# Kernel tuning notes

Hardware: AMD Instinct MI355X
Metric: run time of the kernel (lower is better)

The kernel has to match this reference:

```python
import jax, jax.numpy as jnp
import numpy as np

N = 50000
IN_C, HID_C, CLS_C = 512, 256, 128
E = 800000


def setup_inputs() -> dict:
    key = jax.random.key(0)
    k1, k2, k3, k4, k5, k6 = jax.random.split(key, 6)
    x = jax.random.normal(k1, (N, IN_C), dtype=jnp.float32)
    edge_index = jax.random.randint(k2, (2, E), 0, N, dtype=jnp.int64)
    # GCNConv params (glorot weights, zero bias as in PyG init)
    W1 = jax.random.normal(k3, (IN_C, HID_C), dtype=jnp.float32) * (1.0 / np.sqrt(IN_C))
    b1 = jnp.zeros((HID_C,), dtype=jnp.float32)
    W2 = jax.random.normal(k4, (HID_C, CLS_C), dtype=jnp.float32) * (1.0 / np.sqrt(HID_C))
    b2 = jnp.zeros((CLS_C,), dtype=jnp.float32)
    return {"x": x, "W1": W1, "b1": b1, "W2": W2, "b2": b2, "edge_index": edge_index}


def _norm_edges(edge_index, n):
    # PyG GCNConv: add self-loops, symmetric normalization deg^-1/2
    loops = jnp.arange(n, dtype=edge_index.dtype)
    src = jnp.concatenate([edge_index[0], loops])
    dst = jnp.concatenate([edge_index[1], loops])
    ones = jnp.ones_like(src, dtype=jnp.float32)
    deg = jax.ops.segment_sum(ones, dst, num_segments=n)
    dinv = jnp.where(deg > 0, jax.lax.rsqrt(deg), 0.0)
    norm = dinv[src] * dinv[dst]  # [E+N]
    return src, dst, norm


def _gcn_conv(x, W, b, src, dst, norm, n):
    h = x @ W  # project first (out_channels < in_channels)
    msg = h[src] * norm[:, None]  # gather + scale, [E+N, C]
    out = jax.ops.segment_sum(msg, dst, num_segments=n)  # scatter-add
    return out + b


def reference(x, W1, b1, W2, b2, edge_index):
    n = x.shape[0]
    src, dst, norm = _norm_edges(edge_index, n)
    h = jax.nn.relu(_gcn_conv(x, W1, b1, src, dst, norm, n))
    # dropout p=0.5 is a no-op in eval mode
    out = _gcn_conv(h, W2, b2, src, dst, norm, n)
    return jax.nn.sigmoid(out)
```

## Files before the change

### kernel.cpp

```cpp
#include <hip/hip_runtime.h>

typedef __attribute__((ext_vector_type(8))) short bf16x8;
typedef __attribute__((ext_vector_type(4))) float f32x4;
typedef unsigned short u16;
typedef unsigned int u32;
typedef __attribute__((address_space(1))) const u32 gu32;
typedef __attribute__((address_space(3))) u32 lu32;

__device__ __forceinline__ float bf2f(u16 u) {
  union { u32 i; float f; } c; c.i = ((u32)u) << 16; return c.f;
}
__device__ __forceinline__ u16 f2bf(float f) {
  union { float f; u32 i; } c; c.f = f;
  u32 u = c.i;
  u32 r = (u + 0x7FFFu + ((u >> 16) & 1u)) >> 16;
  return (u16)r;
}

__device__ __forceinline__ void gld16(const void* g, void* l) {
  __builtin_amdgcn_global_load_lds((gu32*)g, (lu32*)l, 16, 0, 0);
}


__global__ void k_init_deg(int* deg, int n) {
  int i = blockIdx.x * 256 + threadIdx.x;
  if (i < n) deg[i] = 1;
}

__global__ void k_count(const int* __restrict__ ei, int* deg, int E) {
  int e = blockIdx.x * 256 + threadIdx.x;
  if (e < E) atomicAdd(&deg[ei[E + e]], 1);
}

__global__ void k_blocksum(const int* __restrict__ deg, int* bsum, int n) {
  __shared__ int s[256];
  int t = threadIdx.x;
  int i = blockIdx.x * 256 + t;
  s[t] = (i < n) ? (deg[i] - 1) : 0;
  __syncthreads();
  for (int o = 128; o > 0; o >>= 1) {
    if (t < o) s[t] += s[t + o];
    __syncthreads();
  }
  if (t == 0) bsum[blockIdx.x] = s[0];
}

__global__ void k_scanb(const int* __restrict__ bsum, int* bofs, int nb) {
  __shared__ int s[256];
  int t = threadIdx.x;
  int v = (t < nb) ? bsum[t] : 0;
  s[t] = v;
  __syncthreads();
  for (int o = 1; o < 256; o <<= 1) {
    int x = (t >= o) ? s[t - o] : 0;
    __syncthreads();
    s[t] += x;
    __syncthreads();
  }
  bofs[t] = s[t] - v;
}

__global__ void k_rowptr(const int* __restrict__ deg, const int* __restrict__ bofs,
                         int* rowptr, int* cursor, float* dinv, int n) {
  __shared__ int s[256];
  int t = threadIdx.x;
  int i = blockIdx.x * 256 + t;
  int d = (i < n) ? deg[i] : 1;
  int v = (i < n) ? (d - 1) : 0;
  s[t] = v;
  __syncthreads();
  for (int o = 1; o < 256; o <<= 1) {
    int x = (t >= o) ? s[t - o] : 0;
    __syncthreads();
    s[t] += x;
    __syncthreads();
  }
  int excl = s[t] - v + bofs[blockIdx.x];
  if (i < n) {
    rowptr[i] = excl;
    cursor[i] = excl;
    dinv[i] = rsqrtf((float)d);
    if (i == n - 1) rowptr[n] = excl + v;
  }
}

__global__ void k_fill(const int* __restrict__ ei, int* cursor,
                       const float* __restrict__ dinv, int2* colw, int E) {
  int e = blockIdx.x * 256 + threadIdx.x;
  if (e >= E) return;
  int s = ei[e];
  int d = ei[E + e];
  int pos = atomicAdd(&cursor[d], 1);
  colw[pos] = make_int2(s, __float_as_int(dinv[s]));
}

__global__ void k_twt(const float* __restrict__ W, u16* __restrict__ Wt, int K, int N) {
  int i = blockIdx.x * 256 + threadIdx.x;
  if (i >= K * N) return;
  int k = i / N, n = i - k * N;
  Wt[n * K + k] = f2bf(W[i]);
}


template <bool AF32, int K, int BM>
__launch_bounds__(256, 4)
__global__ void gemm_kernel(const void* __restrict__ Ap, const u16* __restrict__ Bt,
                            u16* __restrict__ C, int M, int ldc) {
  constexpr int NT = K / 32;
  constexpr int AE = BM * 32;
  constexpr int WROWS = BM / 2;
  constexpr int FI = WROWS / 16;
  constexpr int NJA = BM / 64;
  __shared__ u16 As_[2][AE];
  __shared__ u16 Bs_[2][4096];

  const int tid = threadIdx.x;
  const int lane = tid & 63;
  const int wid = tid >> 6;
  const int wr = wid >> 1, wc = wid & 1;
  const long brow = (long)blockIdx.x * BM;
  const long bcol = (long)blockIdx.y * 128;

  const u16* bgp[2];
  u16* blp[2];
#pragma unroll
  for (int j = 0; j < 2; ++j) {
    int idx = j * 256 + tid;
    int row = idx >> 2;
    int u = (idx & 3) ^ (row & 3);
    bgp[j] = Bt + (bcol + row) * (long)K + u * 8;
    blp[j] = &Bs_[0][idx * 8];
  }

  const float* apf = nullptr;
  int arow = 0, au0 = 0, au1 = 0;
  const u16* agp[NJA];
  u16* alp[NJA];
  if constexpr (AF32) {
    arow = tid >> 1;
    int khalf = tid & 1;
    long grow = brow + arow; if (grow > (long)M - 1) grow = M - 1;
    apf = (const float*)Ap + grow * (long)K + khalf * 16;
    int sw = arow & 3;
    au0 = (2 * khalf) ^ sw;
    au1 = (2 * khalf + 1) ^ sw;
  } else {
#pragma unroll
    for (int j = 0; j < NJA; ++j) {
      int idx = j * 256 + tid;
      int row = idx >> 2;
      int u = (idx & 3) ^ (row & 3);
      long grow = brow + row; if (grow > (long)M - 1) grow = M - 1;
      agp[j] = (const u16*)Ap + grow * (long)K + u * 8;
      alp[j] = &As_[0][idx * 8];
    }
  }

  float4 fa[4];
  auto loadA = [&](int kt) {
    const float4* p = (const float4*)(apf + kt * 32);
#pragma unroll
    for (int i = 0; i < 4; ++i) fa[i] = p[i];
  };
  auto writeA = [&](int buf) {
    union { u32 w[8]; uint4 v[2]; } pk;
    asm("v_cvt_pk_bf16_f32 %0, %1, %2" : "=v"(pk.w[0]) : "v"(fa[0].x), "v"(fa[0].y));
    asm("v_cvt_pk_bf16_f32 %0, %1, %2" : "=v"(pk.w[1]) : "v"(fa[0].z), "v"(fa[0].w));
    asm("v_cvt_pk_bf16_f32 %0, %1, %2" : "=v"(pk.w[2]) : "v"(fa[1].x), "v"(fa[1].y));
    asm("v_cvt_pk_bf16_f32 %0, %1, %2" : "=v"(pk.w[3]) : "v"(fa[1].z), "v"(fa[1].w));
    asm("v_cvt_pk_bf16_f32 %0, %1, %2" : "=v"(pk.w[4]) : "v"(fa[2].x), "v"(fa[2].y));
    asm("v_cvt_pk_bf16_f32 %0, %1, %2" : "=v"(pk.w[5]) : "v"(fa[2].z), "v"(fa[2].w));
    asm("v_cvt_pk_bf16_f32 %0, %1, %2" : "=v"(pk.w[6]) : "v"(fa[3].x), "v"(fa[3].y));
    asm("v_cvt_pk_bf16_f32 %0, %1, %2" : "=v"(pk.w[7]) : "v"(fa[3].z), "v"(fa[3].w));
    *(uint4*)&As_[buf][arow * 32 + au0 * 8] = pk.v[0];
    *(uint4*)&As_[buf][arow * 32 + au1 * 8] = pk.v[1];
  };
  auto stageB = [&](int kt, int buf) {
#pragma unroll
    for (int j = 0; j < 2; ++j) gld16(bgp[j] + kt * 32, blp[j] + buf * 4096);
  };
  auto stageAg = [&](int kt, int buf) {
#pragma unroll
    for (int j = 0; j < NJA; ++j) gld16(agp[j] + kt * 32, alp[j] + buf * AE);
  };

  f32x4 acc[FI][4];
#pragma unroll
  for (int i = 0; i < FI; i++)
#pragma unroll
    for (int j = 0; j < 4; j++) acc[i][j] = (f32x4){0.f, 0.f, 0.f, 0.f};

  if constexpr (AF32) {
    loadA(0);
    stageB(0, 0);
    writeA(0);
  } else {
    stageAg(0, 0);
    stageB(0, 0);
  }
  __syncthreads();

  int cur = 0;
  for (int kt = 0; kt < NT; ++kt) {
    const bool more = (kt + 1 < NT);
    if constexpr (AF32) {
      if (more) { loadA(kt + 1); stageB(kt + 1, cur ^ 1); }
    } else {
      if (more) { stageAg(kt + 1, cur ^ 1); stageB(kt + 1, cur ^ 1); }
    }

    bf16x8 af[FI], bfq[4];
#pragma unroll
    for (int i = 0; i < FI; i++) {
      const int row = wr * WROWS + i * 16 + (lane & 15);
      const int u = (lane >> 4) ^ (row & 3);
      af[i] = *(const bf16x8*)&As_[cur][row * 32 + u * 8];
    }
#pragma unroll
    for (int j = 0; j < 4; j++) {
      const int row = wc * 64 + j * 16 + (lane & 15);
      const int u = (lane >> 4) ^ (row & 3);
      bfq[j] = *(const bf16x8*)&Bs_[cur][row * 32 + u * 8];
    }
#pragma unroll
    for (int i = 0; i < FI; i++)
#pragma unroll
      for (int j = 0; j < 4; j++)
        acc[i][j] = __builtin_amdgcn_mfma_f32_16x16x32_bf16(af[i], bfq[j], acc[i][j], 0, 0, 0);

    if constexpr (AF32) {
      if (more) writeA(cur ^ 1);
    }
    __syncthreads();
    cur ^= 1;
  }

#pragma unroll
  for (int i = 0; i < FI; i++) {
    const long r0 = brow + wr * WROWS + i * 16 + ((lane >> 4) * 4);
#pragma unroll
    for (int j = 0; j < 4; j++) {
      const long cc = bcol + wc * 64 + j * 16 + (lane & 15);
#pragma unroll
      for (int q = 0; q < 4; q++) {
        long r = r0 + q;
        if (r < M) C[r * (long)ldc + cc] = f2bf(acc[i][j][q]);
      }
    }
  }
}


__device__ __forceinline__ float sigmoidf_(float x) { return 1.f / (1.f + __expf(-x)); }

__launch_bounds__(256)
__global__ void agg1(const u16* __restrict__ h0, const int* __restrict__ rowptr,
                     const int2* __restrict__ colw, const float* __restrict__ dinv,
                     const float* __restrict__ b1, u16* __restrict__ h, int n) {
  const int wid = threadIdx.x >> 6, lane = threadIdx.x & 63;
  const int node = blockIdx.x * 4 + wid;
  if (node >= n) return;
  const float di = dinv[node];
  ushort4 sv = ((const ushort4*)(h0 + (size_t)node * 256))[lane];
  float a0 = di * bf2f(sv.x), a1 = di * bf2f(sv.y), a2 = di * bf2f(sv.z), a3 = di * bf2f(sv.w);
  int e = rowptr[node];
  const int r1 = rowptr[node + 1];
  for (; e + 8 <= r1; e += 8) {
    int2 c[8];
#pragma unroll
    for (int q = 0; q < 8; ++q) c[q] = colw[e + q];
    ushort4 v[8];
#pragma unroll
    for (int q = 0; q < 8; ++q)
      v[q] = ((const ushort4*)(h0 + (size_t)c[q].x * 256))[lane];
#pragma unroll
    for (int q = 0; q < 8; ++q) {
      float wv = __int_as_float(c[q].y);
      a0 += wv * bf2f(v[q].x); a1 += wv * bf2f(v[q].y);
      a2 += wv * bf2f(v[q].z); a3 += wv * bf2f(v[q].w);
    }
  }
  for (; e < r1; ++e) {
    int2 c = colw[e];
    float wv = __int_as_float(c.y);
    ushort4 v = ((const ushort4*)(h0 + (size_t)c.x * 256))[lane];
    a0 += wv * bf2f(v.x); a1 += wv * bf2f(v.y); a2 += wv * bf2f(v.z); a3 += wv * bf2f(v.w);
  }
  float4 bb = ((const float4*)b1)[lane];
  a0 = a0 * di + bb.x; a1 = a1 * di + bb.y; a2 = a2 * di + bb.z; a3 = a3 * di + bb.w;
  a0 = fmaxf(a0, 0.f); a1 = fmaxf(a1, 0.f); a2 = fmaxf(a2, 0.f); a3 = fmaxf(a3, 0.f);
  ushort4 o; o.x = f2bf(a0); o.y = f2bf(a1); o.z = f2bf(a2); o.w = f2bf(a3);
  ((ushort4*)(h + (size_t)node * 256))[lane] = o;
}

__launch_bounds__(256)
__global__ void agg2(const u16* __restrict__ h2, const int* __restrict__ rowptr,
                     const int2* __restrict__ colw, const float* __restrict__ dinv,
                     const float* __restrict__ b2, float* __restrict__ out, int n) {
  const int wid = threadIdx.x >> 6, lane = threadIdx.x & 63;
  const int node = blockIdx.x * 4 + wid;
  if (node >= n) return;
  const float di = dinv[node];
  ushort2 sv = ((const ushort2*)(h2 + (size_t)node * 128))[lane];
  float a0 = di * bf2f(sv.x), a1 = di * bf2f(sv.y);
  int e = rowptr[node];
  const int r1 = rowptr[node + 1];
  for (; e + 8 <= r1; e += 8) {
    int2 c[8];
#pragma unroll
    for (int q = 0; q < 8; ++q) c[q] = colw[e + q];
    ushort2 v[8];
#pragma unroll
    for (int q = 0; q < 8; ++q)
      v[q] = ((const ushort2*)(h2 + (size_t)c[q].x * 128))[lane];
#pragma unroll
    for (int q = 0; q < 8; ++q) {
      float wv = __int_as_float(c[q].y);
      a0 += wv * bf2f(v[q].x); a1 += wv * bf2f(v[q].y);
    }
  }
  for (; e < r1; ++e) {
    int2 c = colw[e];
    float wv = __int_as_float(c.y);
    ushort2 v = ((const ushort2*)(h2 + (size_t)c.x * 128))[lane];
    a0 += wv * bf2f(v.x); a1 += wv * bf2f(v.y);
  }
  float2 bb = ((const float2*)b2)[lane];
  float2 o;
  o.x = sigmoidf_(a0 * di + bb.x);
  o.y = sigmoidf_(a1 * di + bb.y);
  ((float2*)(out + (size_t)node * 128))[lane] = o;
}


extern "C" void kernel_launch(void* const* d_in, const int* in_sizes, int n_in,
                              void* d_out, int out_size, void* d_ws, size_t ws_size,
                              hipStream_t stream) {
  const float* x  = (const float*)d_in[0];
  const float* W1 = (const float*)d_in[1];
  const float* b1 = (const float*)d_in[2];
  const float* W2 = (const float*)d_in[3];
  const float* b2 = (const float*)d_in[4];
  const int*   ei = (const int*)d_in[5];

  const int N = in_sizes[0] / 512;
  const int E = in_sizes[5] / 2;
  const int Mpad = (N + 127) & ~127;
  float* outp = (float*)d_out;

  char* w = (char*)d_ws;
  size_t off = 0;
  auto take = [&](size_t bytes) -> void* {
    void* p = w + off;
    off = (off + bytes + 255) & ~(size_t)255;
    return p;
  };
  u16*   h0     = (u16*)take((size_t)Mpad * 256 * 2);
  u16*   hb     = (u16*)take((size_t)Mpad * 256 * 2);
  u16*   h2     = (u16*)take((size_t)Mpad * 128 * 2);
  u16*   W1t    = (u16*)take(256 * 512 * 2);
  u16*   W2t    = (u16*)take(128 * 256 * 2);
  int*   deg    = (int*)take((size_t)N * 4);
  float* dinv   = (float*)take((size_t)N * 4);
  int*   rowptr = (int*)take((size_t)(N + 1) * 4);
  int*   cursor = (int*)take((size_t)N * 4);
  int2*  colw   = (int2*)take((size_t)E * 8);
  int*   bsum   = (int*)take(256 * 4);
  int*   bofs   = (int*)take(256 * 4);
  (void)ws_size; (void)n_in; (void)out_size;

  const int nb = (N + 255) / 256;
  const int eb = (E + 255) / 256;

  k_init_deg<<<nb, 256, 0, stream>>>(deg, N);
  k_count<<<eb, 256, 0, stream>>>(ei, deg, E);
  k_blocksum<<<nb, 256, 0, stream>>>(deg, bsum, N);
  k_scanb<<<1, 256, 0, stream>>>(bsum, bofs, nb);
  k_rowptr<<<nb, 256, 0, stream>>>(deg, bofs, rowptr, cursor, dinv, N);
  k_fill<<<eb, 256, 0, stream>>>(ei, cursor, dinv, colw, E);
  k_twt<<<(512 * 256 + 255) / 256, 256, 0, stream>>>(W1, W1t, 512, 256);
  k_twt<<<(256 * 128 + 255) / 256, 256, 0, stream>>>(W2, W2t, 256, 128);

  dim3 g1(Mpad / 128, 2);
  gemm_kernel<true, 512, 128><<<g1, 256, 0, stream>>>((const void*)x, W1t, h0, N, 256);
  agg1<<<(N + 3) / 4, 256, 0, stream>>>(h0, rowptr, colw, dinv, b1, hb, N);
  dim3 g2(Mpad / 64, 1);
  gemm_kernel<false, 256, 64><<<g2, 256, 0, stream>>>((const void*)hb, W2t, h2, Mpad, 128);
  agg2<<<(N + 3) / 4, 256, 0, stream>>>(h2, rowptr, colw, dinv, b2, outp, N);
}
```

Measured before the change: 252.1 us.

## Stage fp32 A tiles via async global-to-LDS loads and convert at fragment read

The first GEMM now loads fp32 x tiles directly into LDS with global_load_lds and converts them to bf16 when MFMA fragments are read, in place of staging through registers. The k-loop now uses explicit vmcnt waits and raw s_barrier with sched_barrier fences to overlap the next tile's loads with compute. This doubles the A-tile LDS footprint, so launch bounds for that kernel drop to 3 blocks per CU. Smaller changes merge the two weight-transpose kernels, replace the deg init kernel with a memset, and drop the self-loop offset from the degree array.

```diff
diff --git a/kernel.cpp b/kernel.cpp
--- a/kernel.cpp
+++ b/kernel.cpp
@@ -22,11 +22,6 @@
 }
 
 
-__global__ void k_init_deg(int* deg, int n) {
-  int i = blockIdx.x * 256 + threadIdx.x;
-  if (i < n) deg[i] = 1;
-}
-
 __global__ void k_count(const int* __restrict__ ei, int* deg, int E) {
   int e = blockIdx.x * 256 + threadIdx.x;
   if (e < E) atomicAdd(&deg[ei[E + e]], 1);
@@ -36,7 +31,7 @@
   __shared__ int s[256];
   int t = threadIdx.x;
   int i = blockIdx.x * 256 + t;
-  s[t] = (i < n) ? (deg[i] - 1) : 0;
+  s[t] = (i < n) ? deg[i] : 0;
   __syncthreads();
   for (int o = 128; o > 0; o >>= 1) {
     if (t < o) s[t] += s[t + o];
@@ -65,8 +60,7 @@
   __shared__ int s[256];
   int t = threadIdx.x;
   int i = blockIdx.x * 256 + t;
-  int d = (i < n) ? deg[i] : 1;
-  int v = (i < n) ? (d - 1) : 0;
+  int v = (i < n) ? deg[i] : 0;
   s[t] = v;
   __syncthreads();
   for (int o = 1; o < 256; o <<= 1) {
@@ -79,7 +73,7 @@
   if (i < n) {
     rowptr[i] = excl;
     cursor[i] = excl;
-    dinv[i] = rsqrtf((float)d);
+    dinv[i] = rsqrtf((float)(v + 1));
     if (i == n - 1) rowptr[n] = excl + v;
   }
 }
@@ -94,24 +88,34 @@
   colw[pos] = make_int2(s, __float_as_int(dinv[s]));
 }
 
-__global__ void k_twt(const float* __restrict__ W, u16* __restrict__ Wt, int K, int N) {
+__global__ void k_twt2(const float* __restrict__ W1, u16* __restrict__ W1t,
+                       const float* __restrict__ W2, u16* __restrict__ W2t) {
   int i = blockIdx.x * 256 + threadIdx.x;
-  if (i >= K * N) return;
-  int k = i / N, n = i - k * N;
-  Wt[n * K + k] = f2bf(W[i]);
-}
-
-
-template <bool AF32, int K, int BM>
-__launch_bounds__(256, 4)
+  if (i < 512 * 256) {
+    int k = i >> 8, n = i & 255;
+    W1t[n * 512 + k] = f2bf(W1[i]);
+  } else {
+    int j = i - 512 * 256;
+    if (j < 256 * 128) {
+      int k = j >> 7, n = j & 127;
+      W2t[n * 256 + k] = f2bf(W2[j]);
+    }
+  }
+}
+
+
+template <bool AF32, int K, int BM, int MAXB>
+__launch_bounds__(256, MAXB)
 __global__ void gemm_kernel(const void* __restrict__ Ap, const u16* __restrict__ Bt,
                             u16* __restrict__ C, int M, int ldc) {
   constexpr int NT = K / 32;
-  constexpr int AE = BM * 32;
+  constexpr int ABYTES = BM * 32 * (AF32 ? 4 : 2);
+  constexpr int AU16 = ABYTES / 2;
+  constexpr int NJA = ABYTES / 4096;
+  constexpr int S = NJA + 2;
   constexpr int WROWS = BM / 2;
   constexpr int FI = WROWS / 16;
-  constexpr int NJA = BM / 64;
-  __shared__ u16 As_[2][AE];
+  __shared__ u16 As_[2][AU16];
   __shared__ u16 Bs_[2][4096];
 
   const int tid = threadIdx.x;
@@ -121,6 +125,18 @@
   const long brow = (long)blockIdx.x * BM;
   const long bcol = (long)blockIdx.y * 128;
 
+  const char* agp[NJA];
+  char* alp[NJA];
+#pragma unroll
+  for (int j = 0; j < NJA; ++j) {
+    int idx = j * 256 + tid;
+    int row, u;
+    if constexpr (AF32) { row = idx >> 3; u = (idx & 7) ^ (row & 7); }
+    else                { row = idx >> 2; u = (idx & 3) ^ (row & 3); }
+    long grow = brow + row; if (grow > (long)M - 1) grow = M - 1;
+    agp[j] = (const char*)Ap + (grow * (long)K) * (AF32 ? 4 : 2) + u * 16;
+    alp[j] = (char*)&As_[0][0] + idx * 16;
+  }
   const u16* bgp[2];
   u16* blp[2];
 #pragma unroll
@@ -132,57 +148,13 @@
     blp[j] = &Bs_[0][idx * 8];
   }
 
-  const float* apf = nullptr;
-  int arow = 0, au0 = 0, au1 = 0;
-  const u16* agp[NJA];
-  u16* alp[NJA];
-  if constexpr (AF32) {
-    arow = tid >> 1;
-    int khalf = tid & 1;
-    long grow = brow + arow; if (grow > (long)M - 1) grow = M - 1;
-    apf = (const float*)Ap + grow * (long)K + khalf * 16;
-    int sw = arow & 3;
-    au0 = (2 * khalf) ^ sw;
-    au1 = (2 * khalf + 1) ^ sw;
-  } else {
-#pragma unroll
-    for (int j = 0; j < NJA; ++j) {
-      int idx = j * 256 + tid;
-      int row = idx >> 2;
-      int u = (idx & 3) ^ (row & 3);
-      long grow = brow + row; if (grow > (long)M - 1) grow = M - 1;
-      agp[j] = (const u16*)Ap + grow * (long)K + u * 8;
-      alp[j] = &As_[0][idx * 8];
-    }
-  }
-
-  float4 fa[4];
-  auto loadA = [&](int kt) {
-    const float4* p = (const float4*)(apf + kt * 32);
-#pragma unroll
-    for (int i = 0; i < 4; ++i) fa[i] = p[i];
-  };
-  auto writeA = [&](int buf) {
-    union { u32 w[8]; uint4 v[2]; } pk;
-    asm("v_cvt_pk_bf16_f32 %0, %1, %2" : "=v"(pk.w[0]) : "v"(fa[0].x), "v"(fa[0].y));
-    asm("v_cvt_pk_bf16_f32 %0, %1, %2" : "=v"(pk.w[1]) : "v"(fa[0].z), "v"(fa[0].w));
-    asm("v_cvt_pk_bf16_f32 %0, %1, %2" : "=v"(pk.w[2]) : "v"(fa[1].x), "v"(fa[1].y));
-    asm("v_cvt_pk_bf16_f32 %0, %1, %2" : "=v"(pk.w[3]) : "v"(fa[1].z), "v"(fa[1].w));
-    asm("v_cvt_pk_bf16_f32 %0, %1, %2" : "=v"(pk.w[4]) : "v"(fa[2].x), "v"(fa[2].y));
-    asm("v_cvt_pk_bf16_f32 %0, %1, %2" : "=v"(pk.w[5]) : "v"(fa[2].z), "v"(fa[2].w));
-    asm("v_cvt_pk_bf16_f32 %0, %1, %2" : "=v"(pk.w[6]) : "v"(fa[3].x), "v"(fa[3].y));
-    asm("v_cvt_pk_bf16_f32 %0, %1, %2" : "=v"(pk.w[7]) : "v"(fa[3].z), "v"(fa[3].w));
-    *(uint4*)&As_[buf][arow * 32 + au0 * 8] = pk.v[0];
-    *(uint4*)&As_[buf][arow * 32 + au1 * 8] = pk.v[1];
-  };
-  auto stageB = [&](int kt, int buf) {
+  auto stage = [&](int kt, int buf) {
+#pragma unroll
+    for (int j = 0; j < NJA; ++j)
+      gld16(agp[j] + kt * 32 * (AF32 ? 4 : 2), alp[j] + buf * ABYTES);
 #pragma unroll
     for (int j = 0; j < 2; ++j) gld16(bgp[j] + kt * 32, blp[j] + buf * 4096);
   };
-  auto stageAg = [&](int kt, int buf) {
-#pragma unroll
-    for (int j = 0; j < NJA; ++j) gld16(agp[j] + kt * 32, alp[j] + buf * AE);
-  };
 
   f32x4 acc[FI][4];
 #pragma unroll
@@ -190,31 +162,38 @@
 #pragma unroll
     for (int j = 0; j < 4; j++) acc[i][j] = (f32x4){0.f, 0.f, 0.f, 0.f};
 
-  if constexpr (AF32) {
-    loadA(0);
-    stageB(0, 0);
-    writeA(0);
-  } else {
-    stageAg(0, 0);
-    stageB(0, 0);
-  }
-  __syncthreads();
-
+  stage(0, 0);
   int cur = 0;
   for (int kt = 0; kt < NT; ++kt) {
-    const bool more = (kt + 1 < NT);
-    if constexpr (AF32) {
-      if (more) { loadA(kt + 1); stageB(kt + 1, cur ^ 1); }
+    if (kt + 1 < NT) {
+      stage(kt + 1, cur ^ 1);
+      asm volatile("s_waitcnt vmcnt(%0)" :: "n"(S) : "memory");
     } else {
-      if (more) { stageAg(kt + 1, cur ^ 1); stageB(kt + 1, cur ^ 1); }
-    }
+      asm volatile("s_waitcnt vmcnt(0)" ::: "memory");
+    }
+    __builtin_amdgcn_s_barrier();
+    __builtin_amdgcn_sched_barrier(0);
 
     bf16x8 af[FI], bfq[4];
 #pragma unroll
     for (int i = 0; i < FI; i++) {
       const int row = wr * WROWS + i * 16 + (lane & 15);
-      const int u = (lane >> 4) ^ (row & 3);
-      af[i] = *(const bf16x8*)&As_[cur][row * 32 + u * 8];
+      if constexpr (AF32) {
+        const float* bp = (const float*)&As_[cur][0] + row * 32;
+        const int s = row & 7;
+        const int u0 = (lane >> 4) * 2;
+        float4 x0 = *(const float4*)(bp + (u0 ^ s) * 4);
+        float4 x1 = *(const float4*)(bp + ((u0 + 1) ^ s) * 4);
+        union { u32 w[4]; bf16x8 v; } cv;
+        asm("v_cvt_pk_bf16_f32 %0, %1, %2" : "=v"(cv.w[0]) : "v"(x0.x), "v"(x0.y));
+        asm("v_cvt_pk_bf16_f32 %0, %1, %2" : "=v"(cv.w[1]) : "v"(x0.z), "v"(x0.w));
+        asm("v_cvt_pk_bf16_f32 %0, %1, %2" : "=v"(cv.w[2]) : "v"(x1.x), "v"(x1.y));
+        asm("v_cvt_pk_bf16_f32 %0, %1, %2" : "=v"(cv.w[3]) : "v"(x1.z), "v"(x1.w));
+        af[i] = cv.v;
+      } else {
+        const int u = (lane >> 4) ^ (row & 3);
+        af[i] = *(const bf16x8*)&As_[cur][row * 32 + u * 8];
+      }
     }
 #pragma unroll
     for (int j = 0; j < 4; j++) {
@@ -228,10 +207,8 @@
       for (int j = 0; j < 4; j++)
         acc[i][j] = __builtin_amdgcn_mfma_f32_16x16x32_bf16(af[i], bfq[j], acc[i][j], 0, 0, 0);
 
-    if constexpr (AF32) {
-      if (more) writeA(cur ^ 1);
-    }
-    __syncthreads();
+    __builtin_amdgcn_sched_barrier(0);
+    __builtin_amdgcn_s_barrier();
     cur ^= 1;
   }
 
@@ -372,19 +349,18 @@
   const int nb = (N + 255) / 256;
   const int eb = (E + 255) / 256;
 
-  k_init_deg<<<nb, 256, 0, stream>>>(deg, N);
+  hipMemsetAsync(deg, 0, (size_t)N * 4, stream);
   k_count<<<eb, 256, 0, stream>>>(ei, deg, E);
   k_blocksum<<<nb, 256, 0, stream>>>(deg, bsum, N);
   k_scanb<<<1, 256, 0, stream>>>(bsum, bofs, nb);
   k_rowptr<<<nb, 256, 0, stream>>>(deg, bofs, rowptr, cursor, dinv, N);
   k_fill<<<eb, 256, 0, stream>>>(ei, cursor, dinv, colw, E);
-  k_twt<<<(512 * 256 + 255) / 256, 256, 0, stream>>>(W1, W1t, 512, 256);
-  k_twt<<<(256 * 128 + 255) / 256, 256, 0, stream>>>(W2, W2t, 256, 128);
+  k_twt2<<<(512 * 256 + 256 * 128 + 255) / 256, 256, 0, stream>>>(W1, W1t, W2, W2t);
 
   dim3 g1(Mpad / 128, 2);
-  gemm_kernel<true, 512, 128><<<g1, 256, 0, stream>>>((const void*)x, W1t, h0, N, 256);
+  gemm_kernel<true, 512, 128, 3><<<g1, 256, 0, stream>>>((const void*)x, W1t, h0, N, 256);
   agg1<<<(N + 3) / 4, 256, 0, stream>>>(h0, rowptr, colw, dinv, b1, hb, N);
   dim3 g2(Mpad / 64, 1);
-  gemm_kernel<false, 256, 64><<<g2, 256, 0, stream>>>((const void*)hb, W2t, h2, Mpad, 128);
+  gemm_kernel<false, 256, 64, 4><<<g2, 256, 0, stream>>>((const void*)hb, W2t, h2, Mpad, 128);
   agg2<<<(N + 3) / 4, 256, 0, stream>>>(h2, rowptr, colw, dinv, b2, outp, N);
 }
```

New measurement: 253.7 us. No clear change (+0.6%).
